# Optimization experiments

Hardware: AMD Instinct MI355X
Metric: run time of the kernel (lower is better)

Reference implementation:

```python
import jax, jax.numpy as jnp
import numpy as np

LATENT_NUM = 64
N_FEATURES = 10000
BATCH = 4096


def setup_inputs() -> dict:
    key = jax.random.key(0)
    k1, k2 = jax.random.split(key)
    inputs = jax.random.normal(k1, (BATCH, N_FEATURES), dtype=jnp.float32)
    # TruncatedNormal(mean=0, stddev=0.01) approximated with clipped normal
    embedding = jnp.clip(
        jax.random.normal(k2, (N_FEATURES, LATENT_NUM), dtype=jnp.float32) * 0.01,
        -0.02, 0.02,
    )
    return {"inputs": inputs, "embedding": embedding}


def reference(inputs, embedding):
    # Original TF code, per latent dim f:
    #   ex2 = (sum over batch AND features of V[:,f]*X)^2   (reduce_sum w/o axis)
    # Vectorized: t[f] = sum_b (X @ V)[b,f];  q[f] = sum_{b} (X^2 @ V^2)[b,f]
    xv = inputs @ embedding                      # [B, F]
    t = jnp.sum(xv, axis=0)                      # [F]
    q = jnp.sum((inputs * inputs) @ (embedding * embedding), axis=(0, 1))  # scalar
    return 0.5 * (jnp.sum(t * t) - q)
```

## Files before the change

### kernel.cpp

```cpp
#include <hip/hip_runtime.h>

#define NROWS 4096
#define NCOLS 10000
#define NLAT  64
#define NCOLG 2500
#define TPB   256
#define NRC   128
#define RPC   32
#define NSLICE 8
#define CPS   (NRC / NSLICE)
#define NCB   40
#define CPB   250
#define NBLK2 (NCB * NSLICE)

__global__ void colsum_partials(const float* __restrict__ X,
                                float* __restrict__ ps,
                                float* __restrict__ ps2) {
    int jg = blockIdx.x * TPB + threadIdx.x;
    if (jg >= NCOLG) return;
    int r0 = blockIdx.y * RPC;

    float s0 = 0.f, s1 = 0.f, s2 = 0.f, s3 = 0.f;
    float q0 = 0.f, q1 = 0.f, q2 = 0.f, q3 = 0.f;
    const float* base = X + (size_t)r0 * NCOLS + (size_t)jg * 4;
    #pragma unroll 4
    for (int r = 0; r < RPC; ++r) {
        float4 v = *reinterpret_cast<const float4*>(base);
        base += NCOLS;
        s0 += v.x; s1 += v.y; s2 += v.z; s3 += v.w;
        q0 += v.x * v.x; q1 += v.y * v.y; q2 += v.z * v.z; q3 += v.w * v.w;
    }
    size_t o = (size_t)blockIdx.y * NCOLS + (size_t)jg * 4;
    *reinterpret_cast<float4*>(ps  + o) = make_float4(s0, s1, s2, s3);
    *reinterpret_cast<float4*>(ps2 + o) = make_float4(q0, q1, q2, q3);
}

__global__ void fold_q_t(const float* __restrict__ ps,
                         const float* __restrict__ ps2,
                         const float* __restrict__ V,
                         float* __restrict__ tpart,
                         float* __restrict__ qpart) {
    int cb = blockIdx.x;
    int sl = blockIdx.y;
    int j  = threadIdx.x;
    int col = cb * CPB + j;
    bool active = (j < CPB);

    float s = 0.f, s2 = 0.f, q = 0.f;
    if (active) {
        int c0 = sl * CPS;
        #pragma unroll 4
        for (int c = c0; c < c0 + CPS; ++c) {
            s  += ps [(size_t)c * NCOLS + col];
            s2 += ps2[(size_t)c * NCOLS + col];
        }
        float w2 = 0.f;
        const float4* vp = reinterpret_cast<const float4*>(V + (size_t)col * NLAT);
        #pragma unroll
        for (int k = 0; k < NLAT / 4; ++k) {
            float4 v = vp[k];
            w2 += v.x * v.x + v.y * v.y + v.z * v.z + v.w * v.w;
        }
        q = s2 * w2;
    }

    #pragma unroll
    for (int st = 1; st < 64; st <<= 1) q += __shfl_xor(q, st, 64);

    __shared__ float lds_q[4];
    __shared__ float lds_s[TPB];
    __shared__ float lds_t[4][NLAT];
    int lane = threadIdx.x & 63, w = threadIdx.x >> 6;
    if (lane == 0) lds_q[w] = q;
    lds_s[j] = active ? s : 0.f;
    __syncthreads();

    float acc = 0.f;
    const float* Vb = V + (size_t)cb * CPB * NLAT;
    for (int c = w; c < CPB; c += 4)
        acc += lds_s[c] * Vb[(size_t)c * NLAT + lane];
    lds_t[w][lane] = acc;
    __syncthreads();

    int bid = sl * NCB + cb;
    if (threadIdx.x < NLAT)
        tpart[(size_t)bid * NLAT + threadIdx.x] =
            lds_t[0][threadIdx.x] + lds_t[1][threadIdx.x] +
            lds_t[2][threadIdx.x] + lds_t[3][threadIdx.x];
    if (threadIdx.x == 0)
        qpart[bid] = lds_q[0] + lds_q[1] + lds_q[2] + lds_q[3];
}

__global__ void finalize(const float* __restrict__ tpart,
                         const float* __restrict__ qpart,
                         float* __restrict__ out) {
    int f = threadIdx.x;
    float t = 0.f;
    for (int b = 0; b < NBLK2; ++b) t += tpart[(size_t)b * NLAT + f];
    float q = 0.f;
    for (int b = f; b < NBLK2; b += 64) q += qpart[b];
    float tt = t * t;
    #pragma unroll
    for (int st = 1; st < 64; st <<= 1) {
        tt += __shfl_xor(tt, st, 64);
        q  += __shfl_xor(q,  st, 64);
    }
    if (f == 0) out[0] = 0.5f * (tt - q);
}

extern "C" void kernel_launch(void* const* d_in, const int* in_sizes, int n_in,
                              void* d_out, int out_size, void* d_ws, size_t ws_size,
                              hipStream_t stream) {
    const float* X = (const float*)d_in[0];
    const float* V = (const float*)d_in[1];
    float* out = (float*)d_out;

    float* ps    = (float*)d_ws;
    float* ps2   = ps  + (size_t)NRC * NCOLS;
    float* tpart = ps2 + (size_t)NRC * NCOLS;
    float* qpart = tpart + (size_t)NBLK2 * NLAT;

    colsum_partials<<<dim3((NCOLG + TPB - 1) / TPB, NRC), TPB, 0, stream>>>(X, ps, ps2);
    fold_q_t<<<dim3(NCB, NSLICE), TPB, 0, stream>>>(ps, ps2, V, tpart, qpart);
    finalize<<<1, 64, 0, stream>>>(tpart, qpart, out);
}
```

Before: 51.26 us.

## Fuse finalize into fold kernel via last-block atomic counter, double slices

```diff
diff --git a/kernel.cpp b/kernel.cpp
--- a/kernel.cpp
+++ b/kernel.cpp
@@ -7,7 +7,7 @@
 #define TPB   256
 #define NRC   128
 #define RPC   32
-#define NSLICE 8
+#define NSLICE 16
 #define CPS   (NRC / NSLICE)
 #define NCB   40
 #define CPB   250
@@ -15,15 +15,16 @@
 
 __global__ void colsum_partials(const float* __restrict__ X,
                                 float* __restrict__ ps,
-                                float* __restrict__ ps2) {
+                                float* __restrict__ ps2,
+                                unsigned int* __restrict__ counter) {
+    if (blockIdx.x == 0 && blockIdx.y == 0 && threadIdx.x == 0) *counter = 0u;
     int jg = blockIdx.x * TPB + threadIdx.x;
     if (jg >= NCOLG) return;
-    int r0 = blockIdx.y * RPC;
 
     float s0 = 0.f, s1 = 0.f, s2 = 0.f, s3 = 0.f;
     float q0 = 0.f, q1 = 0.f, q2 = 0.f, q3 = 0.f;
-    const float* base = X + (size_t)r0 * NCOLS + (size_t)jg * 4;
-    #pragma unroll 4
+    const float* base = X + (size_t)blockIdx.y * RPC * NCOLS + (size_t)jg * 4;
+    #pragma unroll 8
     for (int r = 0; r < RPC; ++r) {
         float4 v = *reinterpret_cast<const float4*>(base);
         base += NCOLS;
@@ -35,11 +36,12 @@
     *reinterpret_cast<float4*>(ps2 + o) = make_float4(q0, q1, q2, q3);
 }
 
-__global__ void fold_q_t(const float* __restrict__ ps,
-                         const float* __restrict__ ps2,
-                         const float* __restrict__ V,
-                         float* __restrict__ tpart,
-                         float* __restrict__ qpart) {
+__global__ void fold_q_t_final(const float* __restrict__ ps,
+                               const float* __restrict__ ps2,
+                               const float* __restrict__ V,
+                               float* __restrict__ tpT,
+                               unsigned int* __restrict__ counter,
+                               float* __restrict__ out) {
     int cb = blockIdx.x;
     int sl = blockIdx.y;
     int j  = threadIdx.x;
@@ -49,7 +51,7 @@
     float s = 0.f, s2 = 0.f, q = 0.f;
     if (active) {
         int c0 = sl * CPS;
-        #pragma unroll 4
+        #pragma unroll
         for (int c = c0; c < c0 + CPS; ++c) {
             s  += ps [(size_t)c * NCOLS + col];
             s2 += ps2[(size_t)c * NCOLS + col];
@@ -84,28 +86,43 @@
 
     int bid = sl * NCB + cb;
     if (threadIdx.x < NLAT)
-        tpart[(size_t)bid * NLAT + threadIdx.x] =
+        tpT[(size_t)threadIdx.x * NBLK2 + bid] =
             lds_t[0][threadIdx.x] + lds_t[1][threadIdx.x] +
             lds_t[2][threadIdx.x] + lds_t[3][threadIdx.x];
     if (threadIdx.x == 0)
-        qpart[bid] = lds_q[0] + lds_q[1] + lds_q[2] + lds_q[3];
-}
+        tpT[(size_t)NLAT * NBLK2 + bid] = lds_q[0] + lds_q[1] + lds_q[2] + lds_q[3];
 
-__global__ void finalize(const float* __restrict__ tpart,
-                         const float* __restrict__ qpart,
-                         float* __restrict__ out) {
-    int f = threadIdx.x;
-    float t = 0.f;
-    for (int b = 0; b < NBLK2; ++b) t += tpart[(size_t)b * NLAT + f];
-    float q = 0.f;
-    for (int b = f; b < NBLK2; b += 64) q += qpart[b];
-    float tt = t * t;
-    #pragma unroll
-    for (int st = 1; st < 64; st <<= 1) {
-        tt += __shfl_xor(tt, st, 64);
-        q  += __shfl_xor(q,  st, 64);
+    __threadfence();
+    __syncthreads();
+    __shared__ unsigned int is_last;
+    if (threadIdx.x == 0) is_last = (atomicAdd(counter, 1u) == NBLK2 - 1) ? 1u : 0u;
+    __syncthreads();
+    if (!is_last) return;
+    __threadfence();
+
+    int f = threadIdx.x & 63, seg = threadIdx.x >> 6;
+    const float4* row = reinterpret_cast<const float4*>(
+        tpT + (size_t)f * NBLK2 + seg * (NBLK2 / 4));
+    float tf = 0.f;
+    #pragma unroll 8
+    for (int i = 0; i < NBLK2 / 16; ++i) {
+        float4 v = row[i];
+        tf += v.x + v.y + v.z + v.w;
     }
-    if (f == 0) out[0] = 0.5f * (tt - q);
+    __shared__ float red[4][NLAT];
+    red[seg][f] = tf;
+    __syncthreads();
+    if (threadIdx.x < NLAT) {
+        float t = red[0][f] + red[1][f] + red[2][f] + red[3][f];
+        const float* qrow = tpT + (size_t)NLAT * NBLK2;
+        float qf = 0.f;
+        #pragma unroll
+        for (int b = 0; b < NBLK2 / 64; ++b) qf += qrow[f * (NBLK2 / 64) + b];
+        float d = t * t - qf;
+        #pragma unroll
+        for (int st = 1; st < 64; st <<= 1) d += __shfl_xor(d, st, 64);
+        if (f == 0) out[0] = 0.5f * d;
+    }
 }
 
 extern "C" void kernel_launch(void* const* d_in, const int* in_sizes, int n_in,
@@ -117,10 +134,11 @@
 
     float* ps    = (float*)d_ws;
     float* ps2   = ps  + (size_t)NRC * NCOLS;
-    float* tpart = ps2 + (size_t)NRC * NCOLS;
-    float* qpart = tpart + (size_t)NBLK2 * NLAT;
+    float* tpT   = ps2 + (size_t)NRC * NCOLS;
+    unsigned int* counter = (unsigned int*)(tpT + (size_t)(NLAT + 1) * NBLK2);
 
-    colsum_partials<<<dim3((NCOLG + TPB - 1) / TPB, NRC), TPB, 0, stream>>>(X, ps, ps2);
-    fold_q_t<<<dim3(NCB, NSLICE), TPB, 0, stream>>>(ps, ps2, V, tpart, qpart);
-    finalize<<<1, 64, 0, stream>>>(tpart, qpart, out);
+    colsum_partials<<<dim3((NCOLG + TPB - 1) / TPB, NRC), TPB, 0, stream>>>(
+        X, ps, ps2, counter);
+    fold_q_t_final<<<dim3(NCB, NSLICE), TPB, 0, stream>>>(
+        ps, ps2, V, tpT, counter, out);
 }
```

Result: slower. 103.4 us (+101.6%).

## Fuse column-sum and embedding projection into one pass, parallelize finalize

Applied to the files above, without the earlier changes.

```diff
diff --git a/kernel.cpp b/kernel.cpp
--- a/kernel.cpp
+++ b/kernel.cpp
@@ -3,109 +3,103 @@
 #define NROWS 4096
 #define NCOLS 10000
 #define NLAT  64
-#define NCOLG 2500
 #define TPB   256
+#define COLB  1024
+#define NBX   10
 #define NRC   128
 #define RPC   32
-#define NSLICE 8
-#define CPS   (NRC / NSLICE)
-#define NCB   40
-#define CPB   250
-#define NBLK2 (NCB * NSLICE)
+#define NBLK  (NBX * NRC)
+#define TPB2  1024
 
-__global__ void colsum_partials(const float* __restrict__ X,
-                                float* __restrict__ ps,
-                                float* __restrict__ ps2) {
-    int jg = blockIdx.x * TPB + threadIdx.x;
-    if (jg >= NCOLG) return;
-    int r0 = blockIdx.y * RPC;
+__global__ __launch_bounds__(TPB) void pass_x(const float* __restrict__ X,
+                                              const float* __restrict__ V,
+                                              float* __restrict__ tpart,
+                                              float* __restrict__ qpart) {
+    const int bx = blockIdx.x;
+    const int by = blockIdx.y;
+    const int tid = threadIdx.x;
+    const int col0 = bx * COLB;
+    const int jg = col0 + tid * 4;
 
     float s0 = 0.f, s1 = 0.f, s2 = 0.f, s3 = 0.f;
     float q0 = 0.f, q1 = 0.f, q2 = 0.f, q3 = 0.f;
-    const float* base = X + (size_t)r0 * NCOLS + (size_t)jg * 4;
+    if (jg < NCOLS) {
+        const float* p = X + (size_t)by * RPC * NCOLS + jg;
+        #pragma unroll 8
+        for (int r = 0; r < RPC; ++r) {
+            float4 v = *reinterpret_cast<const float4*>(p);
+            p += NCOLS;
+            s0 += v.x; s1 += v.y; s2 += v.z; s3 += v.w;
+            q0 += v.x * v.x; q1 += v.y * v.y; q2 += v.z * v.z; q3 += v.w * v.w;
+        }
+    }
+
+    __shared__ float lds_s [COLB];
+    __shared__ float lds_s2[COLB];
+    *reinterpret_cast<float4*>(&lds_s [tid * 4]) = make_float4(s0, s1, s2, s3);
+    *reinterpret_cast<float4*>(&lds_s2[tid * 4]) = make_float4(q0, q1, q2, q3);
+    __syncthreads();
+
+    const int lane = tid & 63, w = tid >> 6;
+    const int cmax = (NCOLS - col0 < COLB) ? (NCOLS - col0) : COLB;
+    float at = 0.f, aq = 0.f;
     #pragma unroll 4
-    for (int r = 0; r < RPC; ++r) {
-        float4 v = *reinterpret_cast<const float4*>(base);
-        base += NCOLS;
-        s0 += v.x; s1 += v.y; s2 += v.z; s3 += v.w;
-        q0 += v.x * v.x; q1 += v.y * v.y; q2 += v.z * v.z; q3 += v.w * v.w;
-    }
-    size_t o = (size_t)blockIdx.y * NCOLS + (size_t)jg * 4;
-    *reinterpret_cast<float4*>(ps  + o) = make_float4(s0, s1, s2, s3);
-    *reinterpret_cast<float4*>(ps2 + o) = make_float4(q0, q1, q2, q3);
-}
-
-__global__ void fold_q_t(const float* __restrict__ ps,
-                         const float* __restrict__ ps2,
-                         const float* __restrict__ V,
-                         float* __restrict__ tpart,
-                         float* __restrict__ qpart) {
-    int cb = blockIdx.x;
-    int sl = blockIdx.y;
-    int j  = threadIdx.x;
-    int col = cb * CPB + j;
-    bool active = (j < CPB);
-
-    float s = 0.f, s2 = 0.f, q = 0.f;
-    if (active) {
-        int c0 = sl * CPS;
-        #pragma unroll 4
-        for (int c = c0; c < c0 + CPS; ++c) {
-            s  += ps [(size_t)c * NCOLS + col];
-            s2 += ps2[(size_t)c * NCOLS + col];
-        }
-        float w2 = 0.f;
-        const float4* vp = reinterpret_cast<const float4*>(V + (size_t)col * NLAT);
-        #pragma unroll
-        for (int k = 0; k < NLAT / 4; ++k) {
-            float4 v = vp[k];
-            w2 += v.x * v.x + v.y * v.y + v.z * v.z + v.w * v.w;
-        }
-        q = s2 * w2;
+    for (int c = w; c < cmax; c += 4) {
+        float v  = V[(size_t)(col0 + c) * NLAT + lane];
+        float sc = lds_s[c], s2c = lds_s2[c];
+        at = fmaf(sc, v, at);
+        aq = fmaf(s2c, v * v, aq);
     }
 
     #pragma unroll
-    for (int st = 1; st < 64; st <<= 1) q += __shfl_xor(q, st, 64);
+    for (int st = 1; st < 64; st <<= 1) aq += __shfl_xor(aq, st, 64);
 
+    __shared__ float lds_t[4][NLAT];
     __shared__ float lds_q[4];
-    __shared__ float lds_s[TPB];
-    __shared__ float lds_t[4][NLAT];
-    int lane = threadIdx.x & 63, w = threadIdx.x >> 6;
-    if (lane == 0) lds_q[w] = q;
-    lds_s[j] = active ? s : 0.f;
+    if (lane == 0) lds_q[w] = aq;
+    lds_t[w][lane] = at;
     __syncthreads();
 
-    float acc = 0.f;
-    const float* Vb = V + (size_t)cb * CPB * NLAT;
-    for (int c = w; c < CPB; c += 4)
-        acc += lds_s[c] * Vb[(size_t)c * NLAT + lane];
-    lds_t[w][lane] = acc;
-    __syncthreads();
-
-    int bid = sl * NCB + cb;
-    if (threadIdx.x < NLAT)
-        tpart[(size_t)bid * NLAT + threadIdx.x] =
-            lds_t[0][threadIdx.x] + lds_t[1][threadIdx.x] +
-            lds_t[2][threadIdx.x] + lds_t[3][threadIdx.x];
-    if (threadIdx.x == 0)
+    const int bid = by * NBX + bx;
+    if (tid < NLAT)
+        tpart[(size_t)bid * NLAT + tid] =
+            lds_t[0][tid] + lds_t[1][tid] + lds_t[2][tid] + lds_t[3][tid];
+    if (tid == 0)
         qpart[bid] = lds_q[0] + lds_q[1] + lds_q[2] + lds_q[3];
 }
 
-__global__ void finalize(const float* __restrict__ tpart,
-                         const float* __restrict__ qpart,
-                         float* __restrict__ out) {
-    int f = threadIdx.x;
-    float t = 0.f;
-    for (int b = 0; b < NBLK2; ++b) t += tpart[(size_t)b * NLAT + f];
-    float q = 0.f;
-    for (int b = f; b < NBLK2; b += 64) q += qpart[b];
-    float tt = t * t;
+__global__ __launch_bounds__(TPB2) void finalize(const float* __restrict__ tpart,
+                                                 const float* __restrict__ qpart,
+                                                 float* __restrict__ out) {
+    const int tid = threadIdx.x, f = tid & 63, seg = tid >> 6;
+    float tf = 0.f;
+    for (int b = seg; b < NBLK; b += 16)
+        tf += tpart[(size_t)b * NLAT + f];
+    __shared__ float red[16][NLAT];
+    red[seg][f] = tf;
+
+    float qa = 0.f;
+    for (int b = tid; b < NBLK; b += TPB2) qa += qpart[b];
     #pragma unroll
-    for (int st = 1; st < 64; st <<= 1) {
-        tt += __shfl_xor(tt, st, 64);
-        q  += __shfl_xor(q,  st, 64);
+    for (int st = 1; st < 64; st <<= 1) qa += __shfl_xor(qa, st, 64);
+    __shared__ float qr[16];
+    if (f == 0) qr[seg] = qa;
+    __syncthreads();
+
+    if (tid < NLAT) {
+        float t = 0.f;
+        #pragma unroll
+        for (int s = 0; s < 16; ++s) t += red[s][tid];
+        float d = t * t;
+        #pragma unroll
+        for (int st = 1; st < 64; st <<= 1) d += __shfl_xor(d, st, 64);
+        if (tid == 0) {
+            float q = 0.f;
+            #pragma unroll
+            for (int s = 0; s < 16; ++s) q += qr[s];
+            out[0] = 0.5f * (d - q);
+        }
     }
-    if (f == 0) out[0] = 0.5f * (tt - q);
 }
 
 extern "C" void kernel_launch(void* const* d_in, const int* in_sizes, int n_in,
@@ -115,12 +109,9 @@
     const float* V = (const float*)d_in[1];
     float* out = (float*)d_out;
 
-    float* ps    = (float*)d_ws;
-    float* ps2   = ps  + (size_t)NRC * NCOLS;
-    float* tpart = ps2 + (size_t)NRC * NCOLS;
-    float* qpart = tpart + (size_t)NBLK2 * NLAT;
+    float* tpart = (float*)d_ws;
+    float* qpart = tpart + (size_t)NBLK * NLAT;
 
-    colsum_partials<<<dim3((NCOLG + TPB - 1) / TPB, NRC), TPB, 0, stream>>>(X, ps, ps2);
-    fold_q_t<<<dim3(NCB, NSLICE), TPB, 0, stream>>>(ps, ps2, V, tpart, qpart);
-    finalize<<<1, 64, 0, stream>>>(tpart, qpart, out);
+    pass_x<<<dim3(NBX, NRC), TPB, 0, stream>>>(X, V, tpart, qpart);
+    finalize<<<1, TPB2, 0, stream>>>(tpart, qpart, out);
 }
```

Result: slower. 69.63 us (+35.8%).
